# Kernel optimization log

Hardware: AMD Instinct MI355X
Metric: run time of the kernel (lower is better)

The kernel has to match this reference:

```python
import jax, jax.numpy as jnp
import numpy as np

B = 65536
LAYERS = [256, 512, 512, 256]


def setup_inputs() -> dict:
    key = jax.random.key(0)
    ks = jax.random.split(key, 10)
    inp = {"data": jax.random.normal(ks[0], (B, LAYERS[0]), dtype=jnp.float32)}
    for i in range(3):
        n_in, n_out = LAYERS[i], LAYERS[i + 1]
        # link weights ~ U[0,1) like random.random(); bias params[0] zeroed in torch code
        inp[f"W{i+1}"] = jax.random.uniform(ks[1 + 3 * i], (n_in, n_out), dtype=jnp.float32)
        inp[f"b{i+1}"] = jnp.zeros((n_out,), dtype=jnp.float32)
        # per-node activation params a = params[1:6], torch.rand init
        inp[f"a{i+1}"] = jax.random.uniform(ks[2 + 3 * i], (n_out, 5), dtype=jnp.float32)
    return inp


def _act(x, a):
    # x: [B, n], a: [n, 5]; a0*tanh(x)*sin(a1*x+a2) + a3*x + a4  (per-node params broadcast over batch)
    return a[:, 0] * jnp.tanh(x) * jnp.sin(a[:, 1] * x + a[:, 2]) + a[:, 3] * x + a[:, 4]


def reference(data, W1, b1, a1, W2, b2, a2, W3, b3, a3):
    h = _act(data @ W1 + b1, a1)
    h = _act(h @ W2 + b2, a2)
    h = _act(h @ W3 + b3, a3)
    return jax.nn.softmax(h, axis=1)
```

## Files before the change

kernel.cpp:

```cpp
#include <hip/hip_runtime.h>

#define BATCH 65536

typedef float f32x4 __attribute__((ext_vector_type(4)));
typedef _Float16 f16x8 __attribute__((ext_vector_type(8)));

__device__ __forceinline__ void async_ld16(const void* g, void* l) {
  __builtin_amdgcn_global_load_lds(
      (const __attribute__((address_space(1))) void*)g,
      (__attribute__((address_space(3))) void*)l, 16, 0, 0);
}

__device__ __forceinline__ float act_f(float x, float a0, float a1, float a2,
                                       float a3, float a4) {
  float ax = fabsf(x);
  float e = __builtin_amdgcn_exp2f(ax * -2.8853900817779268f);
  float th = (1.0f - e) * __builtin_amdgcn_rcpf(1.0f + e);
  th = copysignf(th, x);
  float arg = fmaf(a1, x, a2);
  float rev = arg * 0.15915494309189535f;
  rev -= floorf(rev);
  float s = __builtin_amdgcn_sinf(rev);
  return fmaf(a3, x, fmaf(a0 * th, s, a4));
}

__global__ __launch_bounds__(256) void splitT_k(const float* __restrict__ W,
                                                _Float16* __restrict__ hi,
                                                _Float16* __restrict__ lo,
                                                int K, int N) {
  const int i = blockIdx.x * 256 + threadIdx.x;
  if (i >= K * N) return;
  const int k = i / N, n = i % N;
  const float w = W[i];
  const _Float16 h = (_Float16)w;
  hi[(size_t)n * K + k] = h;
  lo[(size_t)n * K + k] = (_Float16)(w - (float)h);
}

__device__ __forceinline__ f32x4 mfma3(f16x8 ah, f16x8 al, f16x8 bh, f16x8 bl,
                                       f32x4 c) {
  c = __builtin_amdgcn_mfma_f32_16x16x32_f16(ah, bh, c, 0, 0, 0);
  c = __builtin_amdgcn_mfma_f32_16x16x32_f16(ah, bl, c, 0, 0, 0);
  c = __builtin_amdgcn_mfma_f32_16x16x32_f16(al, bh, c, 0, 0, 0);
  return c;
}

template <bool AF32, bool FINAL>
__global__ __launch_bounds__(256, 4) void gemm_act(
    const float* __restrict__ Af, const _Float16* __restrict__ Ahi,
    const _Float16* __restrict__ Alo, const _Float16* __restrict__ Bhi,
    const _Float16* __restrict__ Blo, const float* __restrict__ bias,
    const float* __restrict__ ap, _Float16* __restrict__ Chi,
    _Float16* __restrict__ Clo, float* __restrict__ Cout, int K, int N) {
  __shared__ __align__(16) _Float16 sA[4096];
  __shared__ __align__(16) _Float16 sB[16384];

  const int tid = threadIdx.x;
  const int wv = tid >> 6;
  const int lane = tid & 63;
  const int wm = wv >> 1, wn = wv & 1;
  const int m16 = lane & 15, quad = lane >> 4;
  const int col0 = blockIdx.x * 256;
  const int row0 = blockIdx.y * 64;

  f32x4 acc[2][8];
  const f32x4 zero = {0.f, 0.f, 0.f, 0.f};
#pragma unroll
  for (int i = 0; i < 2; ++i)
#pragma unroll
    for (int j = 0; j < 8; ++j) acc[i][j] = zero;

  const int nk = K >> 5;
  for (int kt = 0; kt < nk; ++kt) {
    const int k0 = kt << 5;
    if (AF32) {
      float* sAf = (float*)sA;
#pragma unroll
      for (int t = 0; t < 2; ++t) {
        const int c = wv * 2 + t;
        const int r = c * 8 + (lane >> 3);
        const size_t ga = (size_t)(row0 + r) * K + k0 + (lane & 7) * 4;
        async_ld16(Af + ga, (void*)&sAf[c * 256]);
      }
    } else {
      const int r = wv * 16 + (lane >> 2);
      const size_t ga = (size_t)(row0 + r) * K + k0 + (lane & 3) * 8;
      async_ld16(Ahi + ga, (void*)&sA[wv * 512]);
      async_ld16(Alo + ga, (void*)&sA[2048 + wv * 512]);
    }
#pragma unroll
    for (int t = 0; t < 4; ++t) {
      const int c = wv * 4 + t;
      const int col = c * 16 + (lane >> 2);
      const size_t gb = (size_t)(col0 + col) * K + k0 + (lane & 3) * 8;
      async_ld16(Bhi + gb, (void*)&sB[c * 512]);
      async_ld16(Blo + gb, (void*)&sB[8192 + c * 512]);
    }
    __syncthreads();

    f16x8 ah[2], al[2];
#pragma unroll
    for (int tm = 0; tm < 2; ++tm) {
      const int arow = wm * 32 + tm * 16 + m16;
      if (AF32) {
        const float* pa = (const float*)sA + arow * 32 + quad * 8;
        const f32x4 x0 = *(const f32x4*)pa;
        const f32x4 x1 = *(const f32x4*)(pa + 4);
#pragma unroll
        for (int j = 0; j < 4; ++j) {
          const _Float16 h0 = (_Float16)x0[j];
          ah[tm][j] = h0;
          al[tm][j] = (_Float16)(x0[j] - (float)h0);
          const _Float16 h1 = (_Float16)x1[j];
          ah[tm][4 + j] = h1;
          al[tm][4 + j] = (_Float16)(x1[j] - (float)h1);
        }
      } else {
        ah[tm] = *(const f16x8*)&sA[arow * 32 + quad * 8];
        al[tm] = *(const f16x8*)&sA[2048 + arow * 32 + quad * 8];
      }
    }
#pragma unroll
    for (int tn = 0; tn < 8; ++tn) {
      const int bcol = wn * 128 + tn * 16 + m16;
      const f16x8 bh = *(const f16x8*)&sB[bcol * 32 + quad * 8];
      const f16x8 bl = *(const f16x8*)&sB[8192 + bcol * 32 + quad * 8];
#pragma unroll
      for (int tm = 0; tm < 2; ++tm)
        acc[tm][tn] = mfma3(ah[tm], al[tm], bh, bl, acc[tm][tn]);
    }
    __syncthreads();
  }

#pragma unroll
  for (int tn = 0; tn < 8; ++tn) {
    const int col = col0 + wn * 128 + tn * 16 + m16;
    const float bs = bias[col];
    const float p0 = ap[col * 5 + 0];
    const float p1 = ap[col * 5 + 1];
    const float p2 = ap[col * 5 + 2];
    const float p3 = ap[col * 5 + 3];
    const float p4 = ap[col * 5 + 4];
#pragma unroll
    for (int tm = 0; tm < 2; ++tm) {
      const int row = row0 + wm * 32 + tm * 16 + quad * 4;
#pragma unroll
      for (int r = 0; r < 4; ++r) {
        const float y = act_f(acc[tm][tn][r] + bs, p0, p1, p2, p3, p4);
        if (FINAL) {
          Cout[(size_t)(row + r) * 256 + col] = y;
        } else {
          const size_t o = (size_t)(row + r) * N + col;
          const _Float16 h = (_Float16)y;
          Chi[o] = h;
          Clo[o] = (_Float16)(y - (float)h);
        }
      }
    }
  }
}

__global__ __launch_bounds__(256) void softmax_rows(float* __restrict__ io) {
  const int wv = threadIdx.x >> 6, lane = threadIdx.x & 63;
  const size_t row = (size_t)blockIdx.x * 4 + wv;
  f32x4* p = (f32x4*)(io + row * 256);
  f32x4 v = p[lane];
  float m = fmaxf(fmaxf(v[0], v[1]), fmaxf(v[2], v[3]));
#pragma unroll
  for (int off = 32; off > 0; off >>= 1) m = fmaxf(m, __shfl_xor(m, off));
  f32x4 e;
  float s = 0.f;
#pragma unroll
  for (int j = 0; j < 4; ++j) {
    e[j] = __builtin_amdgcn_exp2f((v[j] - m) * 1.4426950408889634f);
    s += e[j];
  }
#pragma unroll
  for (int off = 32; off > 0; off >>= 1) s += __shfl_xor(s, off);
  const float inv = __builtin_amdgcn_rcpf(s);
#pragma unroll
  for (int j = 0; j < 4; ++j) e[j] *= inv;
  p[lane] = e;
}

extern "C" void kernel_launch(void* const* d_in, const int* in_sizes, int n_in,
                              void* d_out, int out_size, void* d_ws,
                              size_t ws_size, hipStream_t stream) {
  const float* data = (const float*)d_in[0];
  const float* W1 = (const float*)d_in[1];
  const float* b1 = (const float*)d_in[2];
  const float* a1 = (const float*)d_in[3];
  const float* W2 = (const float*)d_in[4];
  const float* b2 = (const float*)d_in[5];
  const float* a2 = (const float*)d_in[6];
  const float* W3 = (const float*)d_in[7];
  const float* b3 = (const float*)d_in[8];
  const float* a3 = (const float*)d_in[9];
  float* out = (float*)d_out;

  char* ws = (char*)d_ws;
  const size_t KB = 1024, MB = 1024 * 1024;
  _Float16* w1hi = (_Float16*)(ws + 0 * KB);
  _Float16* w1lo = (_Float16*)(ws + 256 * KB);
  _Float16* w2hi = (_Float16*)(ws + 512 * KB);
  _Float16* w2lo = (_Float16*)(ws + 1024 * KB);
  _Float16* w3hi = (_Float16*)(ws + 1536 * KB);
  _Float16* w3lo = (_Float16*)(ws + 1792 * KB);
  _Float16* h1hi = (_Float16*)(ws + 2 * MB);
  _Float16* h1lo = (_Float16*)(ws + 2 * MB + (size_t)BATCH * 512 * 2);
  _Float16* h2lo = (_Float16*)(ws + 2 * MB + (size_t)BATCH * 512 * 4);
  _Float16* h2hi = (_Float16*)d_out;

  splitT_k<<<(256 * 512 + 255) / 256, 256, 0, stream>>>(W1, w1hi, w1lo, 256, 512);
  splitT_k<<<(512 * 512 + 255) / 256, 256, 0, stream>>>(W2, w2hi, w2lo, 512, 512);
  splitT_k<<<(512 * 256 + 255) / 256, 256, 0, stream>>>(W3, w3hi, w3lo, 512, 256);

  gemm_act<true, false><<<dim3(2, BATCH / 64), 256, 0, stream>>>(
      data, nullptr, nullptr, w1hi, w1lo, b1, a1, h1hi, h1lo, nullptr, 256, 512);
  gemm_act<false, false><<<dim3(2, BATCH / 64), 256, 0, stream>>>(
      nullptr, h1hi, h1lo, w2hi, w2lo, b2, a2, h2hi, h2lo, nullptr, 512, 512);
  gemm_act<false, true><<<dim3(1, BATCH / 64), 256, 0, stream>>>(
      nullptr, h2hi, h2lo, w3hi, w3lo, b3, a3, nullptr, nullptr, out, 512, 256);

  softmax_rows<<<BATCH / 4, 256, 0, stream>>>(out);
}
```

Measured before the change: 454.3 us.

## Fuse all three MLP layers and softmax into one persistent-row-tile kernel

Replaces the three separate GEMM+activation kernels and the softmax kernel with one kernel per 64-row tile. Layer-1 output stays in LDS as swizzled hi/lo fp16, layer 2 is computed in 128-column chunks that feed layer 3 straight away, and the softmax is done in registers with cross-wave reductions through LDS. This removes the global-memory round trips for the large intermediate activations and the extra launches. In exchange it uses 160KB of LDS per block, and weights are read directly from global memory (cache) with no LDS staging, which may limit occupancy and MFMA throughput.

```diff
diff --git a/kernel.cpp b/kernel.cpp
--- a/kernel.cpp
+++ b/kernel.cpp
@@ -4,12 +4,6 @@
 
 typedef float f32x4 __attribute__((ext_vector_type(4)));
 typedef _Float16 f16x8 __attribute__((ext_vector_type(8)));
-
-__device__ __forceinline__ void async_ld16(const void* g, void* l) {
-  __builtin_amdgcn_global_load_lds(
-      (const __attribute__((address_space(1))) void*)g,
-      (__attribute__((address_space(3))) void*)l, 16, 0, 0);
-}
 
 __device__ __forceinline__ float act_f(float x, float a0, float a1, float a2,
                                        float a3, float a4) {
@@ -45,142 +39,250 @@
   return c;
 }
 
-template <bool AF32, bool FINAL>
-__global__ __launch_bounds__(256, 4) void gemm_act(
-    const float* __restrict__ Af, const _Float16* __restrict__ Ahi,
-    const _Float16* __restrict__ Alo, const _Float16* __restrict__ Bhi,
-    const _Float16* __restrict__ Blo, const float* __restrict__ bias,
-    const float* __restrict__ ap, _Float16* __restrict__ Chi,
-    _Float16* __restrict__ Clo, float* __restrict__ Cout, int K, int N) {
-  __shared__ __align__(16) _Float16 sA[4096];
-  __shared__ __align__(16) _Float16 sB[16384];
+__global__ __launch_bounds__(512, 2) void fused_mlp(
+    const float* __restrict__ data, const _Float16* __restrict__ w1h,
+    const _Float16* __restrict__ w1l, const _Float16* __restrict__ w2h,
+    const _Float16* __restrict__ w2l, const _Float16* __restrict__ w3h,
+    const _Float16* __restrict__ w3l, const float* __restrict__ b1,
+    const float* __restrict__ p1, const float* __restrict__ b2,
+    const float* __restrict__ p2, const float* __restrict__ b3,
+    const float* __restrict__ p3, float* __restrict__ out) {
+  __shared__ __align__(16) char smem[163840];
+  char* const h2hB = smem + 131072;
+  char* const h2lB = smem + 147456;
 
   const int tid = threadIdx.x;
   const int wv = tid >> 6;
   const int lane = tid & 63;
-  const int wm = wv >> 1, wn = wv & 1;
-  const int m16 = lane & 15, quad = lane >> 4;
-  const int col0 = blockIdx.x * 256;
-  const int row0 = blockIdx.y * 64;
-
-  f32x4 acc[2][8];
+  const int m16 = lane & 15;
+  const int quad = lane >> 4;
+  const int kq = quad * 8;
+  const int row0 = blockIdx.x * 64;
+
   const f32x4 zero = {0.f, 0.f, 0.f, 0.f};
-#pragma unroll
-  for (int i = 0; i < 2; ++i)
-#pragma unroll
-    for (int j = 0; j < 8; ++j) acc[i][j] = zero;
-
-  const int nk = K >> 5;
-  for (int kt = 0; kt < nk; ++kt) {
-    const int k0 = kt << 5;
-    if (AF32) {
-      float* sAf = (float*)sA;
-#pragma unroll
-      for (int t = 0; t < 2; ++t) {
-        const int c = wv * 2 + t;
-        const int r = c * 8 + (lane >> 3);
-        const size_t ga = (size_t)(row0 + r) * K + k0 + (lane & 7) * 4;
-        async_ld16(Af + ga, (void*)&sAf[c * 256]);
-      }
-    } else {
-      const int r = wv * 16 + (lane >> 2);
-      const size_t ga = (size_t)(row0 + r) * K + k0 + (lane & 3) * 8;
-      async_ld16(Ahi + ga, (void*)&sA[wv * 512]);
-      async_ld16(Alo + ga, (void*)&sA[2048 + wv * 512]);
-    }
-#pragma unroll
-    for (int t = 0; t < 4; ++t) {
-      const int c = wv * 4 + t;
-      const int col = c * 16 + (lane >> 2);
-      const size_t gb = (size_t)(col0 + col) * K + k0 + (lane & 3) * 8;
-      async_ld16(Bhi + gb, (void*)&sB[c * 512]);
-      async_ld16(Blo + gb, (void*)&sB[8192 + c * 512]);
-    }
-    __syncthreads();
-
-    f16x8 ah[2], al[2];
-#pragma unroll
-    for (int tm = 0; tm < 2; ++tm) {
-      const int arow = wm * 32 + tm * 16 + m16;
-      if (AF32) {
-        const float* pa = (const float*)sA + arow * 32 + quad * 8;
+
+  {
+    f32x4 acc[4][4];
+#pragma unroll
+    for (int i = 0; i < 4; ++i)
+#pragma unroll
+      for (int j = 0; j < 4; ++j) acc[i][j] = zero;
+
+#pragma unroll
+    for (int kt = 0; kt < 8; ++kt) {
+      const int k = kt * 32 + kq;
+      f16x8 ah[4], al[4];
+#pragma unroll
+      for (int tm = 0; tm < 4; ++tm) {
+        const float* pa = data + (size_t)(row0 + tm * 16 + m16) * 256 + k;
         const f32x4 x0 = *(const f32x4*)pa;
         const f32x4 x1 = *(const f32x4*)(pa + 4);
 #pragma unroll
         for (int j = 0; j < 4; ++j) {
-          const _Float16 h0 = (_Float16)x0[j];
-          ah[tm][j] = h0;
-          al[tm][j] = (_Float16)(x0[j] - (float)h0);
-          const _Float16 h1 = (_Float16)x1[j];
-          ah[tm][4 + j] = h1;
-          al[tm][4 + j] = (_Float16)(x1[j] - (float)h1);
+          const _Float16 g0 = (_Float16)x0[j];
+          ah[tm][j] = g0;
+          al[tm][j] = (_Float16)(x0[j] - (float)g0);
+          const _Float16 g1 = (_Float16)x1[j];
+          ah[tm][4 + j] = g1;
+          al[tm][4 + j] = (_Float16)(x1[j] - (float)g1);
         }
-      } else {
-        ah[tm] = *(const f16x8*)&sA[arow * 32 + quad * 8];
-        al[tm] = *(const f16x8*)&sA[2048 + arow * 32 + quad * 8];
-      }
-    }
-#pragma unroll
-    for (int tn = 0; tn < 8; ++tn) {
-      const int bcol = wn * 128 + tn * 16 + m16;
-      const f16x8 bh = *(const f16x8*)&sB[bcol * 32 + quad * 8];
-      const f16x8 bl = *(const f16x8*)&sB[8192 + bcol * 32 + quad * 8];
-#pragma unroll
-      for (int tm = 0; tm < 2; ++tm)
-        acc[tm][tn] = mfma3(ah[tm], al[tm], bh, bl, acc[tm][tn]);
+      }
+#pragma unroll
+      for (int tn = 0; tn < 4; ++tn) {
+        const int col = wv * 64 + tn * 16 + m16;
+        const f16x8 bh = *(const f16x8*)(w1h + col * 256 + k);
+        const f16x8 bl = *(const f16x8*)(w1l + col * 256 + k);
+#pragma unroll
+        for (int tm = 0; tm < 4; ++tm)
+          acc[tm][tn] = mfma3(ah[tm], al[tm], bh, bl, acc[tm][tn]);
+      }
+    }
+#pragma unroll
+    for (int tn = 0; tn < 4; ++tn) {
+      const int col = wv * 64 + tn * 16 + m16;
+      const float bs = b1[col];
+      const float q0 = p1[col * 5 + 0], q1 = p1[col * 5 + 1],
+                  q2 = p1[col * 5 + 2], q3 = p1[col * 5 + 3],
+                  q4 = p1[col * 5 + 4];
+#pragma unroll
+      for (int tm = 0; tm < 4; ++tm) {
+#pragma unroll
+        for (int r = 0; r < 4; ++r) {
+          const int row = tm * 16 + quad * 4 + r;
+          const float y = act_f(acc[tm][tn][r] + bs, q0, q1, q2, q3, q4);
+          const _Float16 h = (_Float16)y;
+          const _Float16 l = (_Float16)(y - (float)h);
+          const int off = ((row << 10) + (col << 1)) ^ ((row & 7) << 4);
+          *(_Float16*)(smem + off) = h;
+          *(_Float16*)(smem + 65536 + off) = l;
+        }
+      }
+    }
+  }
+  __syncthreads();
+
+  f32x4 acc3[4][2];
+#pragma unroll
+  for (int i = 0; i < 4; ++i) {
+    acc3[i][0] = zero;
+    acc3[i][1] = zero;
+  }
+
+#pragma unroll 1
+  for (int p = 0; p < 4; ++p) {
+    f32x4 acc2[4];
+#pragma unroll
+    for (int i = 0; i < 4; ++i) acc2[i] = zero;
+    const int colw = p * 128 + wv * 16 + m16;
+#pragma unroll
+    for (int kt = 0; kt < 16; ++kt) {
+      const int k = kt * 32 + kq;
+      const f16x8 bh = *(const f16x8*)(w2h + (size_t)colw * 512 + k);
+      const f16x8 bl = *(const f16x8*)(w2l + (size_t)colw * 512 + k);
+#pragma unroll
+      for (int tm = 0; tm < 4; ++tm) {
+        const int row = tm * 16 + m16;
+        const int off = ((row << 10) + (k << 1)) ^ ((row & 7) << 4);
+        const f16x8 ah = *(const f16x8*)(smem + off);
+        const f16x8 al = *(const f16x8*)(smem + 65536 + off);
+        acc2[tm] = mfma3(ah, al, bh, bl, acc2[tm]);
+      }
     }
     __syncthreads();
-  }
-
-#pragma unroll
-  for (int tn = 0; tn < 8; ++tn) {
-    const int col = col0 + wn * 128 + tn * 16 + m16;
-    const float bs = bias[col];
-    const float p0 = ap[col * 5 + 0];
-    const float p1 = ap[col * 5 + 1];
-    const float p2 = ap[col * 5 + 2];
-    const float p3 = ap[col * 5 + 3];
-    const float p4 = ap[col * 5 + 4];
-#pragma unroll
-    for (int tm = 0; tm < 2; ++tm) {
-      const int row = row0 + wm * 32 + tm * 16 + quad * 4;
-#pragma unroll
-      for (int r = 0; r < 4; ++r) {
-        const float y = act_f(acc[tm][tn][r] + bs, p0, p1, p2, p3, p4);
-        if (FINAL) {
-          Cout[(size_t)(row + r) * 256 + col] = y;
-        } else {
-          const size_t o = (size_t)(row + r) * N + col;
+    {
+      const float bs = b2[colw];
+      const float q0 = p2[colw * 5 + 0], q1 = p2[colw * 5 + 1],
+                  q2 = p2[colw * 5 + 2], q3 = p2[colw * 5 + 3],
+                  q4 = p2[colw * 5 + 4];
+      const int cl = wv * 16 + m16;
+#pragma unroll
+      for (int tm = 0; tm < 4; ++tm) {
+#pragma unroll
+        for (int r = 0; r < 4; ++r) {
+          const int row = tm * 16 + quad * 4 + r;
+          const float y = act_f(acc2[tm][r] + bs, q0, q1, q2, q3, q4);
           const _Float16 h = (_Float16)y;
-          Chi[o] = h;
-          Clo[o] = (_Float16)(y - (float)h);
+          const _Float16 l = (_Float16)(y - (float)h);
+          const int off = ((row << 8) + (cl << 1)) ^ ((row & 7) << 4);
+          *(_Float16*)(h2hB + off) = h;
+          *(_Float16*)(h2lB + off) = l;
         }
       }
     }
-  }
-}
-
-__global__ __launch_bounds__(256) void softmax_rows(float* __restrict__ io) {
-  const int wv = threadIdx.x >> 6, lane = threadIdx.x & 63;
-  const size_t row = (size_t)blockIdx.x * 4 + wv;
-  f32x4* p = (f32x4*)(io + row * 256);
-  f32x4 v = p[lane];
-  float m = fmaxf(fmaxf(v[0], v[1]), fmaxf(v[2], v[3]));
-#pragma unroll
-  for (int off = 32; off > 0; off >>= 1) m = fmaxf(m, __shfl_xor(m, off));
-  f32x4 e;
-  float s = 0.f;
-#pragma unroll
-  for (int j = 0; j < 4; ++j) {
-    e[j] = __builtin_amdgcn_exp2f((v[j] - m) * 1.4426950408889634f);
-    s += e[j];
-  }
-#pragma unroll
-  for (int off = 32; off > 0; off >>= 1) s += __shfl_xor(s, off);
-  const float inv = __builtin_amdgcn_rcpf(s);
-#pragma unroll
-  for (int j = 0; j < 4; ++j) e[j] *= inv;
-  p[lane] = e;
+    __syncthreads();
+#pragma unroll
+    for (int kt = 0; kt < 4; ++kt) {
+      const int kl = kt * 32 + kq;
+      f16x8 ah[4], al[4];
+#pragma unroll
+      for (int tm = 0; tm < 4; ++tm) {
+        const int row = tm * 16 + m16;
+        const int off = ((row << 8) + (kl << 1)) ^ ((row & 7) << 4);
+        ah[tm] = *(const f16x8*)(h2hB + off);
+        al[tm] = *(const f16x8*)(h2lB + off);
+      }
+#pragma unroll
+      for (int tn = 0; tn < 2; ++tn) {
+        const int col = wv * 32 + tn * 16 + m16;
+        const f16x8 bh =
+            *(const f16x8*)(w3h + (size_t)col * 512 + p * 128 + kl);
+        const f16x8 bl =
+            *(const f16x8*)(w3l + (size_t)col * 512 + p * 128 + kl);
+#pragma unroll
+        for (int tm = 0; tm < 4; ++tm)
+          acc3[tm][tn] = mfma3(ah[tm], al[tm], bh, bl, acc3[tm][tn]);
+      }
+    }
+  }
+  __syncthreads();
+
+  float* const red = (float*)(smem + 131072);
+  float* const rowred = (float*)(smem + 131072 + 2048);
+
+  float y[4][2][4];
+#pragma unroll
+  for (int tn = 0; tn < 2; ++tn) {
+    const int col = wv * 32 + tn * 16 + m16;
+    const float bs = b3[col];
+    const float q0 = p3[col * 5 + 0], q1 = p3[col * 5 + 1],
+                q2 = p3[col * 5 + 2], q3 = p3[col * 5 + 3],
+                q4 = p3[col * 5 + 4];
+#pragma unroll
+    for (int tm = 0; tm < 4; ++tm)
+#pragma unroll
+      for (int r = 0; r < 4; ++r)
+        y[tm][tn][r] = act_f(acc3[tm][tn][r] + bs, q0, q1, q2, q3, q4);
+  }
+  float mx[4][4];
+#pragma unroll
+  for (int tm = 0; tm < 4; ++tm)
+#pragma unroll
+    for (int r = 0; r < 4; ++r) {
+      float m = fmaxf(y[tm][0][r], y[tm][1][r]);
+#pragma unroll
+      for (int off = 1; off < 16; off <<= 1) m = fmaxf(m, __shfl_xor(m, off));
+      mx[tm][r] = m;
+    }
+  if (m16 == 0) {
+#pragma unroll
+    for (int tm = 0; tm < 4; ++tm)
+#pragma unroll
+      for (int r = 0; r < 4; ++r)
+        red[wv * 64 + tm * 16 + quad * 4 + r] = mx[tm][r];
+  }
+  __syncthreads();
+  if (tid < 64) {
+    float m = red[tid];
+#pragma unroll
+    for (int w = 1; w < 8; ++w) m = fmaxf(m, red[w * 64 + tid]);
+    rowred[tid] = m;
+  }
+  __syncthreads();
+  float sm[4][4];
+#pragma unroll
+  for (int tm = 0; tm < 4; ++tm)
+#pragma unroll
+    for (int r = 0; r < 4; ++r) {
+      const float m = rowred[tm * 16 + quad * 4 + r];
+      float s = 0.f;
+#pragma unroll
+      for (int tn = 0; tn < 2; ++tn) {
+        const float e =
+            __builtin_amdgcn_exp2f((y[tm][tn][r] - m) * 1.4426950408889634f);
+        y[tm][tn][r] = e;
+        s += e;
+      }
+#pragma unroll
+      for (int off = 1; off < 16; off <<= 1) s += __shfl_xor(s, off);
+      sm[tm][r] = s;
+    }
+  if (m16 == 0) {
+#pragma unroll
+    for (int tm = 0; tm < 4; ++tm)
+#pragma unroll
+      for (int r = 0; r < 4; ++r)
+        red[wv * 64 + tm * 16 + quad * 4 + r] = sm[tm][r];
+  }
+  __syncthreads();
+  if (tid < 64) {
+    float s = red[tid];
+#pragma unroll
+    for (int w = 1; w < 8; ++w) s += red[w * 64 + tid];
+    rowred[tid] = __builtin_amdgcn_rcpf(s);
+  }
+  __syncthreads();
+#pragma unroll
+  for (int tm = 0; tm < 4; ++tm)
+#pragma unroll
+    for (int r = 0; r < 4; ++r) {
+      const int row = tm * 16 + quad * 4 + r;
+      const float inv = rowred[row];
+#pragma unroll
+      for (int tn = 0; tn < 2; ++tn) {
+        const int col = wv * 32 + tn * 16 + m16;
+        out[(size_t)(row0 + row) * 256 + col] = y[tm][tn][r] * inv;
+      }
+    }
 }
 
 extern "C" void kernel_launch(void* const* d_in, const int* in_sizes, int n_in,
@@ -196,31 +298,21 @@
   const float* W3 = (const float*)d_in[7];
   const float* b3 = (const float*)d_in[8];
   const float* a3 = (const float*)d_in[9];
-  float* out = (float*)d_out;
 
   char* ws = (char*)d_ws;
-  const size_t KB = 1024, MB = 1024 * 1024;
-  _Float16* w1hi = (_Float16*)(ws + 0 * KB);
-  _Float16* w1lo = (_Float16*)(ws + 256 * KB);
-  _Float16* w2hi = (_Float16*)(ws + 512 * KB);
-  _Float16* w2lo = (_Float16*)(ws + 1024 * KB);
-  _Float16* w3hi = (_Float16*)(ws + 1536 * KB);
-  _Float16* w3lo = (_Float16*)(ws + 1792 * KB);
-  _Float16* h1hi = (_Float16*)(ws + 2 * MB);
-  _Float16* h1lo = (_Float16*)(ws + 2 * MB + (size_t)BATCH * 512 * 2);
-  _Float16* h2lo = (_Float16*)(ws + 2 * MB + (size_t)BATCH * 512 * 4);
-  _Float16* h2hi = (_Float16*)d_out;
-
-  splitT_k<<<(256 * 512 + 255) / 256, 256, 0, stream>>>(W1, w1hi, w1lo, 256, 512);
-  splitT_k<<<(512 * 512 + 255) / 256, 256, 0, stream>>>(W2, w2hi, w2lo, 512, 512);
-  splitT_k<<<(512 * 256 + 255) / 256, 256, 0, stream>>>(W3, w3hi, w3lo, 512, 256);
-
-  gemm_act<true, false><<<dim3(2, BATCH / 64), 256, 0, stream>>>(
-      data, nullptr, nullptr, w1hi, w1lo, b1, a1, h1hi, h1lo, nullptr, 256, 512);
-  gemm_act<false, false><<<dim3(2, BATCH / 64), 256, 0, stream>>>(
-      nullptr, h1hi, h1lo, w2hi, w2lo, b2, a2, h2hi, h2lo, nullptr, 512, 512);
-  gemm_act<false, true><<<dim3(1, BATCH / 64), 256, 0, stream>>>(
-      nullptr, h2hi, h2lo, w3hi, w3lo, b3, a3, nullptr, nullptr, out, 512, 256);
-
-  softmax_rows<<<BATCH / 4, 256, 0, stream>>>(out);
-}
+  const size_t KB = 1024;
+  _Float16* w1h = (_Float16*)(ws + 0 * KB);
+  _Float16* w1l = (_Float16*)(ws + 256 * KB);
+  _Float16* w2h = (_Float16*)(ws + 512 * KB);
+  _Float16* w2l = (_Float16*)(ws + 1024 * KB);
+  _Float16* w3h = (_Float16*)(ws + 1536 * KB);
+  _Float16* w3l = (_Float16*)(ws + 1792 * KB);
+
+  splitT_k<<<(256 * 512 + 255) / 256, 256, 0, stream>>>(W1, w1h, w1l, 256, 512);
+  splitT_k<<<(512 * 512 + 255) / 256, 256, 0, stream>>>(W2, w2h, w2l, 512, 512);
+  splitT_k<<<(512 * 256 + 255) / 256, 256, 0, stream>>>(W3, w3h, w3l, 512, 256);
+
+  fused_mlp<<<BATCH / 64, 512, 0, stream>>>(data, w1h, w1l, w2h, w2l, w3h, w3l,
+                                            b1, a1, b2, a2, b3, a3,
+                                            (float*)d_out);
+}
```

New measurement: 489.6 us. 1.08x slower.

## Fuse row softmax into final GEMM epilogue and coalesce weight split writes

Applied to the files above, without the earlier changes.

The final layer's GEMM block already holds full 256-column rows for its 64 rows, so the softmax is now computed in the epilogue. Each row's max and sum are reduced with wave shuffles and then combined across the two column waves through shared memory. This removes the separate softmax kernel and its 64MB read-modify-write of the output. The weight split kernel now indexes by the transposed output, so its stores coalesce while its reads stride. In exchange the epilogue gains extra barriers and register pressure.

```diff
diff --git a/kernel.cpp b/kernel.cpp
--- a/kernel.cpp
+++ b/kernel.cpp
@@ -30,11 +30,11 @@
                                                 int K, int N) {
   const int i = blockIdx.x * 256 + threadIdx.x;
   if (i >= K * N) return;
-  const int k = i / N, n = i % N;
-  const float w = W[i];
+  const int n = i / K, k = i % K;
+  const float w = W[(size_t)k * N + n];
   const _Float16 h = (_Float16)w;
-  hi[(size_t)n * K + k] = h;
-  lo[(size_t)n * K + k] = (_Float16)(w - (float)h);
+  hi[i] = h;
+  lo[i] = (_Float16)(w - (float)h);
 }
 
 __device__ __forceinline__ f32x4 mfma3(f16x8 ah, f16x8 al, f16x8 bh, f16x8 bl,
@@ -132,24 +132,91 @@
     __syncthreads();
   }
 
-#pragma unroll
-  for (int tn = 0; tn < 8; ++tn) {
-    const int col = col0 + wn * 128 + tn * 16 + m16;
-    const float bs = bias[col];
-    const float p0 = ap[col * 5 + 0];
-    const float p1 = ap[col * 5 + 1];
-    const float p2 = ap[col * 5 + 2];
-    const float p3 = ap[col * 5 + 3];
-    const float p4 = ap[col * 5 + 4];
-#pragma unroll
-    for (int tm = 0; tm < 2; ++tm) {
-      const int row = row0 + wm * 32 + tm * 16 + quad * 4;
+  if (FINAL) {
+    float* const redf = (float*)sA;
+    float* const rowm = (float*)sA + 128;
+    float* const rowi = (float*)sA + 192;
+#pragma unroll
+    for (int tn = 0; tn < 8; ++tn) {
+      const int col = col0 + wn * 128 + tn * 16 + m16;
+      const float bs = bias[col];
+      const float p0 = ap[col * 5 + 0];
+      const float p1 = ap[col * 5 + 1];
+      const float p2 = ap[col * 5 + 2];
+      const float p3 = ap[col * 5 + 3];
+      const float p4 = ap[col * 5 + 4];
+#pragma unroll
+      for (int tm = 0; tm < 2; ++tm)
+#pragma unroll
+        for (int r = 0; r < 4; ++r)
+          acc[tm][tn][r] = act_f(acc[tm][tn][r] + bs, p0, p1, p2, p3, p4);
+    }
+#pragma unroll
+    for (int tm = 0; tm < 2; ++tm)
 #pragma unroll
       for (int r = 0; r < 4; ++r) {
-        const float y = act_f(acc[tm][tn][r] + bs, p0, p1, p2, p3, p4);
-        if (FINAL) {
-          Cout[(size_t)(row + r) * 256 + col] = y;
-        } else {
+        float m = acc[tm][0][r];
+#pragma unroll
+        for (int tn = 1; tn < 8; ++tn) m = fmaxf(m, acc[tm][tn][r]);
+#pragma unroll
+        for (int off = 1; off < 16; off <<= 1) m = fmaxf(m, __shfl_xor(m, off));
+        if (m16 == 0) {
+          const int rowl = wm * 32 + tm * 16 + quad * 4 + r;
+          redf[wn * 64 + rowl] = m;
+        }
+      }
+    __syncthreads();
+    if (tid < 64) rowm[tid] = fmaxf(redf[tid], redf[64 + tid]);
+    __syncthreads();
+#pragma unroll
+    for (int tm = 0; tm < 2; ++tm)
+#pragma unroll
+      for (int r = 0; r < 4; ++r) {
+        const int rowl = wm * 32 + tm * 16 + quad * 4 + r;
+        const float m = rowm[rowl];
+        float s = 0.f;
+#pragma unroll
+        for (int tn = 0; tn < 8; ++tn) {
+          const float e = __builtin_amdgcn_exp2f((acc[tm][tn][r] - m) *
+                                                 1.4426950408889634f);
+          acc[tm][tn][r] = e;
+          s += e;
+        }
+#pragma unroll
+        for (int off = 1; off < 16; off <<= 1) s += __shfl_xor(s, off);
+        if (m16 == 0) redf[wn * 64 + rowl] = s;
+      }
+    __syncthreads();
+    if (tid < 64) rowi[tid] = __builtin_amdgcn_rcpf(redf[tid] + redf[64 + tid]);
+    __syncthreads();
+#pragma unroll
+    for (int tm = 0; tm < 2; ++tm)
+#pragma unroll
+      for (int r = 0; r < 4; ++r) {
+        const int rowl = wm * 32 + tm * 16 + quad * 4 + r;
+        const float inv = rowi[rowl];
+#pragma unroll
+        for (int tn = 0; tn < 8; ++tn) {
+          const int col = col0 + wn * 128 + tn * 16 + m16;
+          Cout[(size_t)(row0 + rowl) * 256 + col] = acc[tm][tn][r] * inv;
+        }
+      }
+  } else {
+#pragma unroll
+    for (int tn = 0; tn < 8; ++tn) {
+      const int col = col0 + wn * 128 + tn * 16 + m16;
+      const float bs = bias[col];
+      const float p0 = ap[col * 5 + 0];
+      const float p1 = ap[col * 5 + 1];
+      const float p2 = ap[col * 5 + 2];
+      const float p3 = ap[col * 5 + 3];
+      const float p4 = ap[col * 5 + 4];
+#pragma unroll
+      for (int tm = 0; tm < 2; ++tm) {
+        const int row = row0 + wm * 32 + tm * 16 + quad * 4;
+#pragma unroll
+        for (int r = 0; r < 4; ++r) {
+          const float y = act_f(acc[tm][tn][r] + bs, p0, p1, p2, p3, p4);
           const size_t o = (size_t)(row + r) * N + col;
           const _Float16 h = (_Float16)y;
           Chi[o] = h;
@@ -158,29 +225,6 @@
       }
     }
   }
-}
-
-__global__ __launch_bounds__(256) void softmax_rows(float* __restrict__ io) {
-  const int wv = threadIdx.x >> 6, lane = threadIdx.x & 63;
-  const size_t row = (size_t)blockIdx.x * 4 + wv;
-  f32x4* p = (f32x4*)(io + row * 256);
-  f32x4 v = p[lane];
-  float m = fmaxf(fmaxf(v[0], v[1]), fmaxf(v[2], v[3]));
-#pragma unroll
-  for (int off = 32; off > 0; off >>= 1) m = fmaxf(m, __shfl_xor(m, off));
-  f32x4 e;
-  float s = 0.f;
-#pragma unroll
-  for (int j = 0; j < 4; ++j) {
-    e[j] = __builtin_amdgcn_exp2f((v[j] - m) * 1.4426950408889634f);
-    s += e[j];
-  }
-#pragma unroll
-  for (int off = 32; off > 0; off >>= 1) s += __shfl_xor(s, off);
-  const float inv = __builtin_amdgcn_rcpf(s);
-#pragma unroll
-  for (int j = 0; j < 4; ++j) e[j] *= inv;
-  p[lane] = e;
 }
 
 extern "C" void kernel_launch(void* const* d_in, const int* in_sizes, int n_in,
@@ -221,6 +265,4 @@
       nullptr, h1hi, h1lo, w2hi, w2lo, b2, a2, h2hi, h2lo, nullptr, 512, 512);
   gemm_act<false, true><<<dim3(1, BATCH / 64), 256, 0, stream>>>(
       nullptr, h2hi, h2lo, w3hi, w3lo, b3, a3, nullptr, nullptr, out, 512, 256);
-
-  softmax_rows<<<BATCH / 4, 256, 0, stream>>>(out);
-}
+}
```

Result: faster. 427.2 us (-6.0%).
